# Performance work log

Hardware: AMD Instinct MI355X
Metric: run time of the kernel (lower is better)

## Reference

```python
import jax, jax.numpy as jnp
import numpy as np

B, C, H, W = 4, 512, 64, 64
KEY_DIM, VALUE_DIM = 512, 512


def setup_inputs() -> dict:
    key = jax.random.key(0)
    k1, k2, k3, k4 = jax.random.split(key, 4)
    s = 1.0 / np.sqrt(C).astype(np.float32)
    x = jax.random.normal(k1, (B, C, H, W), jnp.float32)
    # torch nn.Linear weights have shape (out_features, in_features)
    Wk = jax.random.normal(k2, (KEY_DIM, C), jnp.float32) * s
    Wq = jax.random.normal(k3, (KEY_DIM, C), jnp.float32) * s
    Wv = jax.random.normal(k4, (VALUE_DIM, C), jnp.float32) * s
    return {"x": x, "Wk": Wk, "Wq": Wq, "Wv": Wv}


def reference(x, Wk, Wq, Wv):
    b, c, h, w = x.shape
    kd = Wk.shape[0]
    n = h * w
    # (b,c,h,w) -> (b, n, c) tokens, matching transpose+flatten in the original
    xt = x.transpose(0, 2, 3, 1).reshape(b, n, c)
    q = xt @ Wq.T  # (b, n, kd)
    k = xt @ Wk.T  # (b, n, kd)
    v = xt @ Wv.T  # (b, n, vd)
    scaling = np.sqrt(float(kd)).astype(np.float32)
    scores = jax.nn.softmax(jnp.einsum('bnd,bmd->bnm', q, k) / scaling, axis=-1)
    # original: output[j] = sum_i values[i] * scores[j, i]  ==  scores @ V
    out = jnp.einsum('bnm,bmv->bnv', scores, v)  # (b, n, vd)
    # original scores_out: sum over dim=0 (query index) of the (n, n) score matrix
    scores_out = scores.sum(axis=1).reshape(b, 1, h, w)
    out = out.reshape(b, h, w, -1).transpose(0, 3, 1, 2)  # (b, vd, h, w)
    return out, scores_out
```

## Files before the change

### kernel.cpp

```cpp
#include <hip/hip_runtime.h>


typedef short bf16x8 __attribute__((ext_vector_type(8)));
typedef float f32x4 __attribute__((ext_vector_type(4)));

#define NTOK 4096
#define DDIM 512
#define NB   4

__device__ __forceinline__ unsigned short f32_bf16(float f) {
  union { float f; unsigned u; } v; v.f = f;
  unsigned r = v.u + 0x7FFFu + ((v.u >> 16) & 1u);
  return (unsigned short)(r >> 16);
}

__device__ __forceinline__ float bf16_f32(short s) {
  union { unsigned u; float f; } v;
  v.u = ((unsigned)(unsigned short)s) << 16;
  return v.f;
}

__global__ __launch_bounds__(256, 4) void qkv_proj(
    const float* __restrict__ x,
    const float* __restrict__ Wq,
    const float* __restrict__ Wk,
    const float* __restrict__ Wv,
    unsigned short* __restrict__ Qt,
    unsigned short* __restrict__ Kt,
    unsigned short* __restrict__ Vt)
{
  const int nt0 = blockIdx.x * 64;
  const int d0  = blockIdx.y * 64;
  const int b   = blockIdx.z;
  const int tid = threadIdx.x;
  const int wave = tid >> 6;
  const int lane = tid & 63;
  const int l15  = lane & 15;
  const int quad = lane >> 4;

  __shared__ __align__(16) unsigned short Xt[64 * 40];
  __shared__ __align__(16) unsigned short Wl[3][64 * 40];

  f32x4 aq[4], ak[4], av[4];
#pragma unroll
  for (int i = 0; i < 4; ++i) {
    aq[i] = (f32x4){0.f,0.f,0.f,0.f};
    ak[i] = (f32x4){0.f,0.f,0.f,0.f};
    av[i] = (f32x4){0.f,0.f,0.f,0.f};
  }

  const float* xb = x + (size_t)b * DDIM * NTOK + nt0;
  const int xn  = tid & 63;
  const int xc8 = tid >> 6;
  const int wc8 = tid & 3;
  const int wdd = tid >> 2;

  for (int cc = 0; cc < DDIM; cc += 32) {
    __syncthreads();
    {
      bf16x8 t;
#pragma unroll
      for (int j = 0; j < 8; ++j)
        t[j] = (short)f32_bf16(xb[(size_t)(cc + xc8 * 8 + j) * NTOK + xn]);
      *(bf16x8*)(&Xt[xn * 40 + xc8 * 8]) = t;
    }
    {
      const float* wsrc[3] = {Wq, Wk, Wv};
#pragma unroll
      for (int m = 0; m < 3; ++m) {
        const float* src = wsrc[m] + (size_t)(d0 + wdd) * DDIM + cc + wc8 * 8;
        bf16x8 t;
#pragma unroll
        for (int j = 0; j < 8; ++j) t[j] = (short)f32_bf16(src[j]);
        *(bf16x8*)(&Wl[m][wdd * 40 + wc8 * 8]) = t;
      }
    }
    __syncthreads();

    bf16x8 xa  = *(const bf16x8*)(&Xt[(wave * 16 + l15) * 40 + quad * 8]);
    bf16x8 wva = *(const bf16x8*)(&Wl[2][(wave * 16 + l15) * 40 + quad * 8]);
#pragma unroll
    for (int nt = 0; nt < 4; ++nt) {
      bf16x8 wqf = *(const bf16x8*)(&Wl[0][(nt * 16 + l15) * 40 + quad * 8]);
      bf16x8 wkf = *(const bf16x8*)(&Wl[1][(nt * 16 + l15) * 40 + quad * 8]);
      bf16x8 xbf = *(const bf16x8*)(&Xt[(nt * 16 + l15) * 40 + quad * 8]);
      aq[nt] = __builtin_amdgcn_mfma_f32_16x16x32_bf16(xa,  wqf, aq[nt], 0, 0, 0);
      ak[nt] = __builtin_amdgcn_mfma_f32_16x16x32_bf16(xa,  wkf, ak[nt], 0, 0, 0);
      av[nt] = __builtin_amdgcn_mfma_f32_16x16x32_bf16(wva, xbf, av[nt], 0, 0, 0);
    }
  }

#pragma unroll
  for (int nt = 0; nt < 4; ++nt) {
#pragma unroll
    for (int r = 0; r < 4; ++r) {
      const int tokq = nt0 + wave * 16 + quad * 4 + r;
      const int dq   = d0 + nt * 16 + l15;
      Qt[((size_t)b * NTOK + tokq) * DDIM + dq] = f32_bf16(aq[nt][r]);
      Kt[((size_t)b * NTOK + tokq) * DDIM + dq] = f32_bf16(ak[nt][r]);
      const int dblk  = (d0 >> 4) + wave;
      const int ic    = (nt0 >> 5) + (nt >> 1);
      const int laneV = ((nt & 1) * 2 + (l15 >> 3)) * 16 + quad * 4 + r;
      Vt[(size_t)b * DDIM * NTOK +
         ((size_t)(dblk * 128 + ic) * 64 + laneV) * 8 + (l15 & 7)] =
          f32_bf16(av[nt][r]);
    }
  }
}

#define BK   64
#define DSUB 256
#define KROW 264
#define SCALE 0.044194173824159216f

__device__ __forceinline__ void stage_k(const unsigned short* __restrict__ src,
                                        unsigned short* __restrict__ Klds,
                                        int tid, int dsi) {
#pragma unroll
  for (int it = 0; it < 8; ++it) {
    const int li = tid + it * 256;
    const int ri = li >> 5;
    const int c8 = li & 31;
    *(bf16x8*)(&Klds[ri * KROW + c8 * 8]) =
        *(const bf16x8*)(src + (size_t)ri * DDIM + dsi * DSUB + c8 * 8);
  }
}

__global__ __launch_bounds__(256, 4) void attn_lsum_p(
    const unsigned short* __restrict__ Qt,
    const unsigned short* __restrict__ Kt,
    unsigned short* __restrict__ Pt,
    float* __restrict__ lsum_g)
{
  const int q0 = blockIdx.x * 64;
  const int k0 = blockIdx.y * (NTOK / 4);
  const int b  = blockIdx.z;
  const int tid = threadIdx.x;
  const int wave = tid >> 6;
  const int lane = tid & 63;
  const int l15  = lane & 15;
  const int quad = lane >> 4;

  __shared__ __align__(16) unsigned short Klds[BK * KROW];

  bf16x8 qf[16];
  {
    const unsigned short* qp =
        Qt + ((size_t)b * NTOK + q0 + wave * 16 + l15) * DDIM + quad * 8;
#pragma unroll
    for (int dc = 0; dc < 16; ++dc) qf[dc] = *(const bf16x8*)(qp + dc * 32);
  }

  const unsigned short* kb = Kt + (size_t)b * NTOK * DDIM;
  unsigned short* Pq = Pt + (size_t)b * NTOK * NTOK + (size_t)(q0 >> 6) * 262144;
  float ls[4] = {0.f, 0.f, 0.f, 0.f};

  for (int kc = 0; kc < (NTOK / 4) / BK; ++kc) {
    const int i0 = k0 + kc * BK;
    const unsigned short* ksrc = kb + (size_t)i0 * DDIM;
    f32x4 sacc[4];
#pragma unroll
    for (int i = 0; i < 4; ++i) sacc[i] = (f32x4){0.f,0.f,0.f,0.f};
#pragma unroll
    for (int dsi = 0; dsi < 2; ++dsi) {
      __syncthreads();
      stage_k(ksrc, Klds, tid, dsi);
      __syncthreads();
#pragma unroll
      for (int dc = 0; dc < 8; ++dc) {
        const int ko = dc * 32 + quad * 8;
        const bf16x8 a = qf[dsi * 8 + dc];
#pragma unroll
        for (int nt = 0; nt < 4; ++nt) {
          bf16x8 kf = *(const bf16x8*)(&Klds[(nt * 16 + l15) * KROW + ko]);
          sacc[nt] = __builtin_amdgcn_mfma_f32_16x16x32_bf16(a, kf, sacc[nt], 0, 0, 0);
        }
      }
    }
#pragma unroll
    for (int nt = 0; nt < 4; ++nt) {
      const int ic    = (i0 >> 5) + (nt >> 1);
      const int laneP = ((nt & 1) * 2 + (l15 >> 3)) * 16 + quad * 4;
#pragma unroll
      for (int r = 0; r < 4; ++r) {
        const float e = __expf(sacc[nt][r] * SCALE);
        ls[r] += e;
        Pq[((size_t)(ic * 4 + wave) * 64 + laneP + r) * 8 + (l15 & 7)] = f32_bf16(e);
      }
    }
  }

#pragma unroll
  for (int r = 0; r < 4; ++r) {
    float v = ls[r];
    v += __shfl_xor(v, 1);
    v += __shfl_xor(v, 2);
    v += __shfl_xor(v, 4);
    v += __shfl_xor(v, 8);
    if (l15 == 0)
      unsafeAtomicAdd(&lsum_g[(size_t)b * NTOK + q0 + wave * 16 + quad * 4 + r], v);
  }
}

__global__ __launch_bounds__(256, 2) void attn_pv(
    const unsigned short* __restrict__ Pt,
    const unsigned short* __restrict__ Vt,
    const float* __restrict__ lsum_g,
    float* __restrict__ out)
{
  const int q0b   = blockIdx.x;
  const int dpart = blockIdx.y;
  const int b     = blockIdx.z;
  const int tid  = threadIdx.x;
  const int wave = tid >> 6;
  const int lane = tid & 63;
  const int l15  = lane & 15;
  const int quad = lane >> 4;

  const int dblk0 = dpart * 16 + wave * 4;
  const unsigned short* Pq =
      Pt + (size_t)b * NTOK * NTOK + (size_t)q0b * 262144 + lane * 8;
  const unsigned short* Vb =
      Vt + (size_t)b * DDIM * NTOK + lane * 8;

  float rlv[4];
#pragma unroll
  for (int nt = 0; nt < 4; ++nt)
    rlv[nt] = 1.0f / lsum_g[(size_t)b * NTOK + q0b * 64 + nt * 16 + l15];

  f32x4 o[4][4];
#pragma unroll
  for (int i = 0; i < 4; ++i)
#pragma unroll
    for (int j = 0; j < 4; ++j) o[i][j] = (f32x4){0.f,0.f,0.f,0.f};

  bf16x8 pc[4], vc[4], pn[4], vn[4];
#pragma unroll
  for (int nt = 0; nt < 4; ++nt)
    pc[nt] = *(const bf16x8*)(Pq + (size_t)nt * 512);
#pragma unroll
  for (int mt = 0; mt < 4; ++mt)
    vc[mt] = *(const bf16x8*)(Vb + (size_t)(dblk0 + mt) * 65536);

#pragma unroll 2
  for (int ic = 0; ic < 127; ++ic) {
#pragma unroll
    for (int nt = 0; nt < 4; ++nt)
      pn[nt] = *(const bf16x8*)(Pq + (size_t)(ic + 1) * 2048 + (size_t)nt * 512);
#pragma unroll
    for (int mt = 0; mt < 4; ++mt)
      vn[mt] = *(const bf16x8*)(Vb + (size_t)(dblk0 + mt) * 65536 + (size_t)(ic + 1) * 512);
#pragma unroll
    for (int mt = 0; mt < 4; ++mt)
#pragma unroll
      for (int nt = 0; nt < 4; ++nt)
        o[mt][nt] = __builtin_amdgcn_mfma_f32_16x16x32_bf16(vc[mt], pc[nt], o[mt][nt], 0, 0, 0);
#pragma unroll
    for (int nt = 0; nt < 4; ++nt) pc[nt] = pn[nt];
#pragma unroll
    for (int mt = 0; mt < 4; ++mt) vc[mt] = vn[mt];
  }
#pragma unroll
  for (int mt = 0; mt < 4; ++mt)
#pragma unroll
    for (int nt = 0; nt < 4; ++nt)
      o[mt][nt] = __builtin_amdgcn_mfma_f32_16x16x32_bf16(vc[mt], pc[nt], o[mt][nt], 0, 0, 0);

  float* ob = out + ((size_t)b * DDIM + dpart * 256 + wave * 64) * NTOK + q0b * 64;
#pragma unroll
  for (int mt = 0; mt < 4; ++mt)
#pragma unroll
    for (int nt = 0; nt < 4; ++nt)
#pragma unroll
      for (int r = 0; r < 4; ++r)
        ob[(size_t)(mt * 16 + quad * 4 + r) * NTOK + nt * 16 + l15] =
            o[mt][nt][r] * rlv[nt];
}

__global__ __launch_bounds__(256, 4) void colsum_k(
    const unsigned short* __restrict__ Pt,
    const float* __restrict__ lsum_g,
    float* __restrict__ scores_out)
{
  const int ic = blockIdx.x;
  const int b  = blockIdx.y;
  const int tid = threadIdx.x;
  const int wave = tid >> 6;
  const int lane = tid & 63;
  const int l15  = lane & 15;
  const int quad = lane >> 4;

  __shared__ float red[4][32];

  const unsigned short* Pb = Pt + (size_t)b * NTOK * NTOK + (size_t)ic * 2048 + lane * 8;
  const float* lb = lsum_g + (size_t)b * NTOK;

  float acc[8];
#pragma unroll
  for (int j = 0; j < 8; ++j) acc[j] = 0.f;

  for (int q0b = wave; q0b < 64; q0b += 4) {
    const unsigned short* src = Pb + (size_t)q0b * 262144;
#pragma unroll
    for (int nt = 0; nt < 4; ++nt) {
      const bf16x8 p = *(const bf16x8*)(src + (size_t)nt * 512);
      const float rl = 1.0f / lb[q0b * 64 + nt * 16 + l15];
#pragma unroll
      for (int j = 0; j < 8; ++j) acc[j] = fmaf(bf16_f32(p[j]), rl, acc[j]);
    }
  }
#pragma unroll
  for (int j = 0; j < 8; ++j) {
    float v = acc[j];
    v += __shfl_xor(v, 1);
    v += __shfl_xor(v, 2);
    v += __shfl_xor(v, 4);
    v += __shfl_xor(v, 8);
    acc[j] = v;
  }
  if (l15 == 0) {
#pragma unroll
    for (int j = 0; j < 8; ++j) red[wave][quad * 8 + j] = acc[j];
  }
  __syncthreads();
  if (tid < 32)
    scores_out[(size_t)b * NTOK + ic * 32 + tid] =
        red[0][tid] + red[1][tid] + red[2][tid] + red[3][tid];
}

extern "C" void kernel_launch(void* const* d_in, const int* in_sizes, int n_in,
                              void* d_out, int out_size, void* d_ws, size_t ws_size,
                              hipStream_t stream) {
  const float* x  = (const float*)d_in[0];
  const float* Wk = (const float*)d_in[1];
  const float* Wq = (const float*)d_in[2];
  const float* Wv = (const float*)d_in[3];

  float* out = (float*)d_out;
  float* scores_out = out + (size_t)NB * DDIM * NTOK;

  const size_t mat_elems = (size_t)NB * NTOK * DDIM;
  unsigned short* Qt = (unsigned short*)d_ws;
  unsigned short* Kt = Qt + mat_elems;
  unsigned short* Vt = Kt + mat_elems;
  float* lbuf = (float*)(Vt + mat_elems);
  unsigned short* Pt = (unsigned short*)(lbuf + (size_t)NB * NTOK);

  hipMemsetAsync(lbuf, 0, (size_t)NB * NTOK * sizeof(float), stream);

  dim3 g1(NTOK / 64, DDIM / 64, NB);
  qkv_proj<<<g1, 256, 0, stream>>>(x, Wq, Wk, Wv, Qt, Kt, Vt);

  dim3 g2(NTOK / 64, 4, NB);
  attn_lsum_p<<<g2, 256, 0, stream>>>(Qt, Kt, Pt, lbuf);

  dim3 g3(NTOK / 64, 2, NB);
  attn_pv<<<g3, 256, 0, stream>>>(Pt, Vt, lbuf, out);

  dim3 g4(128, NB);
  colsum_k<<<g4, 256, 0, stream>>>(Pt, lbuf, scores_out);
}
```

Before: 411.3 us.

## Store K in MFMA fragment layout and stream it from global with register prefetch

The QKV projection now writes K directly in a pre-swizzled MFMA fragment layout. The QK^T/exp kernel can then load K fragments straight into registers from global memory with software double-buffering, instead of staging K tiles through LDS behind two barriers per chunk. Q is staged once into LDS in fragment order and shared across waves. Each block covers 32 queries while each wave owns a separate key range, so the per-chunk __syncthreads are gone. The trade-offs are more global K traffic per block, since K is no longer shared via LDS, higher register pressure (occupancy hint lowered to 3), and a changed grid shape.

```diff
diff --git a/kernel.cpp b/kernel.cpp
--- a/kernel.cpp
+++ b/kernel.cpp
@@ -26,7 +26,7 @@
     const float* __restrict__ Wk,
     const float* __restrict__ Wv,
     unsigned short* __restrict__ Qt,
-    unsigned short* __restrict__ Kt,
+    unsigned short* __restrict__ Kf,
     unsigned short* __restrict__ Vt)
 {
   const int nt0 = blockIdx.x * 64;
@@ -97,7 +97,13 @@
       const int tokq = nt0 + wave * 16 + quad * 4 + r;
       const int dq   = d0 + nt * 16 + l15;
       Qt[((size_t)b * NTOK + tokq) * DDIM + dq] = f32_bf16(aq[nt][r]);
-      Kt[((size_t)b * NTOK + tokq) * DDIM + dq] = f32_bf16(ak[nt][r]);
+      {
+        const int kblk  = (nt0 >> 4) + wave;
+        const int dc    = (d0 >> 5) + (nt >> 1);
+        const int laneK = ((nt & 1) * 2 + (l15 >> 3)) * 16 + quad * 4 + r;
+        Kf[((size_t)(b * 256 + kblk) * 16 + dc) * 512 + laneK * 8 + (l15 & 7)] =
+            f32_bf16(ak[nt][r]);
+      }
       const int dblk  = (d0 >> 4) + wave;
       const int ic    = (nt0 >> 5) + (nt >> 1);
       const int laneV = ((nt & 1) * 2 + (l15 >> 3)) * 16 + quad * 4 + r;
@@ -108,98 +114,108 @@
   }
 }
 
-#define BK   64
-#define DSUB 256
-#define KROW 264
 #define SCALE 0.044194173824159216f
 
-__device__ __forceinline__ void stage_k(const unsigned short* __restrict__ src,
-                                        unsigned short* __restrict__ Klds,
-                                        int tid, int dsi) {
-#pragma unroll
-  for (int it = 0; it < 8; ++it) {
-    const int li = tid + it * 256;
-    const int ri = li >> 5;
-    const int c8 = li & 31;
-    *(bf16x8*)(&Klds[ri * KROW + c8 * 8]) =
-        *(const bf16x8*)(src + (size_t)ri * DDIM + dsi * DSUB + c8 * 8);
-  }
-}
-
-__global__ __launch_bounds__(256, 4) void attn_lsum_p(
+__global__ __launch_bounds__(256, 3) void attn_lsum_p(
     const unsigned short* __restrict__ Qt,
-    const unsigned short* __restrict__ Kt,
+    const unsigned short* __restrict__ Kf,
     unsigned short* __restrict__ Pt,
     float* __restrict__ lsum_g)
 {
-  const int q0 = blockIdx.x * 64;
-  const int k0 = blockIdx.y * (NTOK / 4);
+  const int qb = blockIdx.x;
+  const int kp = blockIdx.y;
   const int b  = blockIdx.z;
-  const int tid = threadIdx.x;
+  const int tid  = threadIdx.x;
   const int wave = tid >> 6;
   const int lane = tid & 63;
   const int l15  = lane & 15;
   const int quad = lane >> 4;
-
-  __shared__ __align__(16) unsigned short Klds[BK * KROW];
-
-  bf16x8 qf[16];
+  const int q0   = qb * 32;
+
+  __shared__ __align__(16) unsigned short Qlds[2 * 16 * 64 * 8];
+
   {
-    const unsigned short* qp =
-        Qt + ((size_t)b * NTOK + q0 + wave * 16 + l15) * DDIM + quad * 8;
-#pragma unroll
-    for (int dc = 0; dc < 16; ++dc) qf[dc] = *(const bf16x8*)(qp + dc * 32);
-  }
-
-  const unsigned short* kb = Kt + (size_t)b * NTOK * DDIM;
+    const int q  = tid >> 3;
+    const int dg = tid & 7;
+    const unsigned short* src = Qt + ((size_t)b * NTOK + q0 + q) * DDIM;
+#pragma unroll
+    for (int u = 0; u < 8; ++u) {
+      const int d = u * 64 + dg * 8;
+      bf16x8 t = *(const bf16x8*)(src + d);
+      *(bf16x8*)&Qlds[((((q >> 4) * 16 + (d >> 5)) * 64) +
+                       ((d >> 3) & 3) * 16 + (q & 15)) * 8] = t;
+    }
+  }
+  __syncthreads();
+
+  const unsigned short* kfb = Kf + (size_t)b * NTOK * DDIM;
+  const int kb0 = kp * 128 + wave * 32;
   unsigned short* Pq = Pt + (size_t)b * NTOK * NTOK + (size_t)(q0 >> 6) * 262144;
-  float ls[4] = {0.f, 0.f, 0.f, 0.f};
-
-  for (int kc = 0; kc < (NTOK / 4) / BK; ++kc) {
-    const int i0 = k0 + kc * BK;
-    const unsigned short* ksrc = kb + (size_t)i0 * DDIM;
-    f32x4 sacc[4];
-#pragma unroll
-    for (int i = 0; i < 4; ++i) sacc[i] = (f32x4){0.f,0.f,0.f,0.f};
-#pragma unroll
-    for (int dsi = 0; dsi < 2; ++dsi) {
-      __syncthreads();
-      stage_k(ksrc, Klds, tid, dsi);
-      __syncthreads();
-#pragma unroll
-      for (int dc = 0; dc < 8; ++dc) {
-        const int ko = dc * 32 + quad * 8;
-        const bf16x8 a = qf[dsi * 8 + dc];
-#pragma unroll
-        for (int nt = 0; nt < 4; ++nt) {
-          bf16x8 kf = *(const bf16x8*)(&Klds[(nt * 16 + l15) * KROW + ko]);
-          sacc[nt] = __builtin_amdgcn_mfma_f32_16x16x32_bf16(a, kf, sacc[nt], 0, 0, 0);
-        }
-      }
-    }
-#pragma unroll
-    for (int nt = 0; nt < 4; ++nt) {
-      const int ic    = (i0 >> 5) + (nt >> 1);
-      const int laneP = ((nt & 1) * 2 + (l15 >> 3)) * 16 + quad * 4;
-#pragma unroll
-      for (int r = 0; r < 4; ++r) {
-        const float e = __expf(sacc[nt][r] * SCALE);
-        ls[r] += e;
-        Pq[((size_t)(ic * 4 + wave) * 64 + laneP + r) * 8 + (l15 & 7)] = f32_bf16(e);
-      }
-    }
-  }
-
-#pragma unroll
-  for (int r = 0; r < 4; ++r) {
-    float v = ls[r];
-    v += __shfl_xor(v, 1);
-    v += __shfl_xor(v, 2);
-    v += __shfl_xor(v, 4);
-    v += __shfl_xor(v, 8);
-    if (l15 == 0)
-      unsafeAtomicAdd(&lsum_g[(size_t)b * NTOK + q0 + wave * 16 + quad * 4 + r], v);
-  }
+  const int ntP0 = (q0 >> 4) & 3;
+
+  float ls[2][4] = {{0.f,0.f,0.f,0.f},{0.f,0.f,0.f,0.f}};
+
+  bf16x8 kA[8], kB[8];
+  {
+    const unsigned short* p0 = kfb + (size_t)kb0 * 8192 + lane * 8;
+#pragma unroll
+    for (int dc = 0; dc < 8; ++dc) kA[dc] = *(const bf16x8*)(p0 + dc * 512);
+  }
+
+  for (int kb = 0; kb < 32; ++kb) {
+    const int kabs = kb0 + kb;
+    const unsigned short* pb = kfb + (size_t)kabs * 8192 + lane * 8;
+#pragma unroll
+    for (int dc = 0; dc < 8; ++dc) kB[dc] = *(const bf16x8*)(pb + (8 + dc) * 512);
+
+    f32x4 s0 = (f32x4){0.f,0.f,0.f,0.f};
+    f32x4 s1 = (f32x4){0.f,0.f,0.f,0.f};
+#pragma unroll
+    for (int dc = 0; dc < 8; ++dc) {
+      bf16x8 qa0 = *(const bf16x8*)&Qlds[(dc * 64 + lane) * 8];
+      bf16x8 qa1 = *(const bf16x8*)&Qlds[((16 + dc) * 64 + lane) * 8];
+      s0 = __builtin_amdgcn_mfma_f32_16x16x32_bf16(qa0, kA[dc], s0, 0, 0, 0);
+      s1 = __builtin_amdgcn_mfma_f32_16x16x32_bf16(qa1, kA[dc], s1, 0, 0, 0);
+    }
+    if (kb < 31) {
+      const unsigned short* pn = kfb + (size_t)(kabs + 1) * 8192 + lane * 8;
+#pragma unroll
+      for (int dc = 0; dc < 8; ++dc) kA[dc] = *(const bf16x8*)(pn + dc * 512);
+    }
+#pragma unroll
+    for (int dc = 0; dc < 8; ++dc) {
+      bf16x8 qa0 = *(const bf16x8*)&Qlds[((8 + dc) * 64 + lane) * 8];
+      bf16x8 qa1 = *(const bf16x8*)&Qlds[((24 + dc) * 64 + lane) * 8];
+      s0 = __builtin_amdgcn_mfma_f32_16x16x32_bf16(qa0, kB[dc], s0, 0, 0, 0);
+      s1 = __builtin_amdgcn_mfma_f32_16x16x32_bf16(qa1, kB[dc], s1, 0, 0, 0);
+    }
+
+    const int ic    = kabs >> 1;
+    const int lt_hi = ((kabs & 1) * 2 + (l15 >> 3)) * 16;
+    const int jj    = l15 & 7;
+#pragma unroll
+    for (int r = 0; r < 4; ++r) {
+      const float e0 = __expf(s0[r] * SCALE);
+      const float e1 = __expf(s1[r] * SCALE);
+      ls[0][r] += e0;
+      ls[1][r] += e1;
+      Pq[((size_t)(ic * 4 + ntP0) * 64 + lt_hi + quad * 4 + r) * 8 + jj] = f32_bf16(e0);
+      Pq[((size_t)(ic * 4 + ntP0 + 1) * 64 + lt_hi + quad * 4 + r) * 8 + jj] = f32_bf16(e1);
+    }
+  }
+
+#pragma unroll
+  for (int qt = 0; qt < 2; ++qt)
+#pragma unroll
+    for (int r = 0; r < 4; ++r) {
+      float v = ls[qt][r];
+      v += __shfl_xor(v, 1);
+      v += __shfl_xor(v, 2);
+      v += __shfl_xor(v, 4);
+      v += __shfl_xor(v, 8);
+      if (l15 == 0)
+        unsafeAtomicAdd(&lsum_g[(size_t)b * NTOK + q0 + qt * 16 + quad * 4 + r], v);
+    }
 }
 
 __global__ __launch_bounds__(256, 2) void attn_pv(
@@ -341,18 +357,18 @@
 
   const size_t mat_elems = (size_t)NB * NTOK * DDIM;
   unsigned short* Qt = (unsigned short*)d_ws;
-  unsigned short* Kt = Qt + mat_elems;
-  unsigned short* Vt = Kt + mat_elems;
+  unsigned short* Kf = Qt + mat_elems;
+  unsigned short* Vt = Kf + mat_elems;
   float* lbuf = (float*)(Vt + mat_elems);
   unsigned short* Pt = (unsigned short*)(lbuf + (size_t)NB * NTOK);
 
   hipMemsetAsync(lbuf, 0, (size_t)NB * NTOK * sizeof(float), stream);
 
   dim3 g1(NTOK / 64, DDIM / 64, NB);
-  qkv_proj<<<g1, 256, 0, stream>>>(x, Wq, Wk, Wv, Qt, Kt, Vt);
-
-  dim3 g2(NTOK / 64, 4, NB);
-  attn_lsum_p<<<g2, 256, 0, stream>>>(Qt, Kt, Pt, lbuf);
+  qkv_proj<<<g1, 256, 0, stream>>>(x, Wq, Wk, Wv, Qt, Kf, Vt);
+
+  dim3 g2(NTOK / 32, 2, NB);
+  attn_lsum_p<<<g2, 256, 0, stream>>>(Qt, Kf, Pt, lbuf);
 
   dim3 g3(NTOK / 64, 2, NB);
   attn_pv<<<g3, 256, 0, stream>>>(Pt, Vt, lbuf, out);
```

New measurement: 480.7 us. 1.17x slower.
